# Kernel tuning notes

Hardware: AMD Instinct MI355X
Metric: run time of the kernel (lower is better)

Reference implementation:

```python
import jax, jax.numpy as jnp
import numpy as np

N_USERS = 100000
N_ITEMS = 50000
D = 64
N_LAYERS = 3
N_NODES = N_USERS + N_ITEMS + 1  # item table has padding row
N_EDGES = 4800000


def setup_inputs() -> dict:
    key = jax.random.key(0)
    k1, k2, k3, k4, k5 = jax.random.split(key, 5)
    user_emb = jax.random.normal(k1, (N_USERS, D), dtype=jnp.float32)
    item_emb = jax.random.normal(k2, (N_ITEMS + 1, D), dtype=jnp.float32)
    vals = jax.random.uniform(k3, (N_EDGES,), dtype=jnp.float32)
    rows = jax.random.randint(k4, (N_EDGES,), 0, N_NODES, dtype=jnp.int64)
    cols = jax.random.randint(k5, (N_EDGES,), 0, N_NODES, dtype=jnp.int64)
    return {"user_emb": user_emb, "item_emb": item_emb, "vals": vals,
            "rows": rows, "cols": cols}


def _spmm(rows, cols, vals, h):
    # y[r] = sum_{e: rows[e]==r} vals[e] * h[cols[e]]
    gathered = vals[:, None] * h[cols]                     # [E, D]
    return jax.ops.segment_sum(gathered, rows, num_segments=N_NODES)


def reference(user_emb, item_emb, vals, rows, cols):
    ego = jnp.concatenate([user_emb, item_emb], axis=0)    # [N, D]
    layer_embeddings = [ego]
    h = ego
    for _ in range(N_LAYERS):
        h = _spmm(rows, cols, vals, h)
        layer_embeddings.append(h)
    h_sum = jnp.stack(layer_embeddings, axis=0).sum(axis=0)
    return (h_sum, *layer_embeddings)
```

## Files before the change

### kernel.cpp

```cpp
#include <hip/hip_runtime.h>
#include <hip/hip_fp16.h>

#define N_USERS 100000
#define N_ITEMS 50000
#define DIM     64
#define N_NODES (N_USERS + N_ITEMS + 1)
#define N_EDGES 4800000

static constexpr long long NF = (long long)N_NODES * DIM;

#define NCB      256
#define CB_ROWS  586
#define CHUNK_E  8192
#define BINA_T   256
#define NCHUNK   ((N_EDGES + CHUNK_E - 1) / CHUNK_E)
#define PB_T     1024

__device__ __forceinline__ uint2 pack_half4(float4 s) {
    uint2 pk;
    *(__half2*)&pk.x = __float22half2_rn(make_float2(s.x, s.y));
    *(__half2*)&pk.y = __float22half2_rn(make_float2(s.z, s.w));
    return pk;
}

__global__ void concat16_kernel(const float4* __restrict__ user,
                                const float4* __restrict__ item,
                                float4* __restrict__ ego,
                                uint2* __restrict__ ego16) {
    int i = blockIdx.x * blockDim.x + threadIdx.x;
    const int userF4 = N_USERS * DIM / 4;
    const int totF4  = (int)(NF / 4);
    if (i < totF4) {
        float4 v = (i < userF4) ? user[i] : item[i - userF4];
        ego[i]   = v;
        ego16[i] = pack_half4(v);
    }
}

__global__ void concat_kernel(const float4* __restrict__ user,
                              const float4* __restrict__ item,
                              float4* __restrict__ ego) {
    int i = blockIdx.x * blockDim.x + threadIdx.x;
    const int userF4 = N_USERS * DIM / 4;
    const int totF4  = (int)(NF / 4);
    if (i < userF4)      ego[i] = user[i];
    else if (i < totF4)  ego[i] = item[i - userF4];
}

__global__ void __launch_bounds__(BINA_T)
binA_count_kernel(const int* __restrict__ rows, int* __restrict__ cnt) {
    __shared__ int hist[NCB];
    int t = threadIdx.x;
    int base = blockIdx.x * CHUNK_E;
    int nend = N_EDGES - base; if (nend > CHUNK_E) nend = CHUNK_E;
    hist[t] = 0;
    __syncthreads();
    for (int i = t; i < nend; i += BINA_T)
        atomicAdd(&hist[rows[base + i] / CB_ROWS], 1);
    __syncthreads();
    cnt[blockIdx.x * NCB + t] = hist[t];
}

__global__ void __launch_bounds__(BINA_T)
binA_scan_kernel(int* __restrict__ cnt, int* __restrict__ stored) {
    __shared__ int lds[BINA_T];
    int b = blockIdx.x, t = threadIdx.x;
    int w0 = 3 * t;
    int v0 = (w0     < NCHUNK) ? cnt[(w0    ) * NCB + b] : 0;
    int v1 = (w0 + 1 < NCHUNK) ? cnt[(w0 + 1) * NCB + b] : 0;
    int v2 = (w0 + 2 < NCHUNK) ? cnt[(w0 + 2) * NCB + b] : 0;
    lds[t] = v0 + v1 + v2;
    __syncthreads();
    for (int off = 1; off < BINA_T; off <<= 1) {
        int x = lds[t];
        int y = (t >= off) ? lds[t - off] : 0;
        __syncthreads();
        lds[t] = x + y;
        __syncthreads();
    }
    int excl = (t == 0) ? 0 : lds[t - 1];
    if (w0     < NCHUNK) cnt[(w0    ) * NCB + b] = excl;
    if (w0 + 1 < NCHUNK) cnt[(w0 + 1) * NCB + b] = excl + v0;
    if (w0 + 2 < NCHUNK) cnt[(w0 + 2) * NCB + b] = excl + v0 + v1;
    if (t == BINA_T - 1) stored[b] = lds[BINA_T - 1];
}

__global__ void __launch_bounds__(NCB)
cb_scan_kernel(const int* __restrict__ stored, int* __restrict__ csr_base,
               int* __restrict__ row_ptr) {
    __shared__ int lds[NCB];
    int t = threadIdx.x;
    lds[t] = stored[t];
    __syncthreads();
    for (int off = 1; off < NCB; off <<= 1) {
        int x = lds[t];
        int y = (t >= off) ? lds[t - off] : 0;
        __syncthreads();
        lds[t] = x + y;
        __syncthreads();
    }
    csr_base[t] = (t == 0) ? 0 : lds[t - 1];
    if (t == 0) { csr_base[NCB] = lds[NCB - 1]; row_ptr[N_NODES] = N_EDGES; }
}

__global__ void __launch_bounds__(BINA_T)
binA_write_kernel(const int* __restrict__ rows, const int* __restrict__ cols,
                  const float* __restrict__ vals,
                  const int* __restrict__ cnt, const int* __restrict__ csr_base,
                  uint2* __restrict__ tmp) {
    __shared__ int offs[NCB];
    int t = threadIdx.x;
    int base = blockIdx.x * CHUNK_E;
    int nend = N_EDGES - base; if (nend > CHUNK_E) nend = CHUNK_E;
    offs[t] = csr_base[t] + cnt[blockIdx.x * NCB + t];
    __syncthreads();
    for (int i = t; i < nend; i += BINA_T) {
        int e = base + i;
        int r = rows[e];
        unsigned c = (unsigned)cols[e];
        unsigned v = __float_as_uint(vals[e]);
        int b = r / CB_ROWS;
        int p = atomicAdd(&offs[b], 1);
        tmp[p] = make_uint2(((unsigned)(r - b * CB_ROWS) << 18) | c, v);
    }
}

__global__ void __launch_bounds__(PB_T)
passB_kernel(const int* __restrict__ csr_base, const uint2* __restrict__ tmp,
             uint2* __restrict__ edges, int* __restrict__ row_ptr) {
    __shared__ int sdeg[PB_T];
    __shared__ int scur[CB_ROWS];
    int b = blockIdx.x, t = threadIdx.x;
    int cb = csr_base[b];
    int n  = csr_base[b + 1] - cb;
    const uint2* tb = tmp + cb;
    sdeg[t] = 0;
    __syncthreads();
    for (int i = t; i < n; i += PB_T)
        atomicAdd(&sdeg[tb[i].x >> 18], 1);
    __syncthreads();
    for (int off = 1; off < PB_T; off <<= 1) {
        int x = sdeg[t];
        int y = (t >= off) ? sdeg[t - off] : 0;
        __syncthreads();
        sdeg[t] = x + y;
        __syncthreads();
    }
    int excl = (t == 0) ? 0 : sdeg[t - 1];
    int gr = b * CB_ROWS + t;
    if (t < CB_ROWS && gr < N_NODES) {
        row_ptr[gr] = cb + excl;
        scur[t] = cb + excl;
    }
    __syncthreads();
    for (int i = t; i < n; i += PB_T) {
        uint2 ed = tb[i];
        int p = atomicAdd(&scur[ed.x >> 18], 1);
        edges[p] = make_uint2(ed.x & 0x3FFFFu, ed.y);
    }
}

__device__ __forceinline__ void fma4(float4& a, float w, float4 v) {
    a.x += w * v.x; a.y += w * v.y; a.z += w * v.z; a.w += w * v.w;
}
__device__ __forceinline__ void fma16(float4& a, float w, uint2 u) {
    float2 lo = __half22float2(*(const __half2*)&u.x);
    float2 hi = __half22float2(*(const __half2*)&u.y);
    a.x += w * lo.x; a.y += w * lo.y; a.z += w * hi.x; a.w += w * hi.y;
}

__global__ void __launch_bounds__(256)
spmm16_kernel(const int* __restrict__ row_ptr,
              const uint2* __restrict__ edges,
              const uint2* __restrict__ hin16,
              float* __restrict__ hout,
              uint2* __restrict__ hout16) {
    int wave = (blockIdx.x * blockDim.x + threadIdx.x) >> 6;
    int lane = threadIdx.x & 63;
    if (wave >= N_NODES) return;
    int g  = lane >> 4;
    int dq = lane & 15;
    int start = row_ptr[wave];
    int end   = row_ptr[wave + 1];
    float4 a0 = make_float4(0.f, 0.f, 0.f, 0.f);
    float4 a1 = a0, a2 = a0, a3 = a0;
    int e = start;
    for (; e + 16 <= end; e += 16) {
        uint2 e0 = edges[e + g];
        uint2 e1 = edges[e + 4 + g];
        uint2 e2 = edges[e + 8 + g];
        uint2 e3 = edges[e + 12 + g];
        uint2 v0 = hin16[(int)e0.x * 16 + dq];
        uint2 v1 = hin16[(int)e1.x * 16 + dq];
        uint2 v2 = hin16[(int)e2.x * 16 + dq];
        uint2 v3 = hin16[(int)e3.x * 16 + dq];
        fma16(a0, __uint_as_float(e0.y), v0);
        fma16(a1, __uint_as_float(e1.y), v1);
        fma16(a2, __uint_as_float(e2.y), v2);
        fma16(a3, __uint_as_float(e3.y), v3);
    }
    for (; e < end; e += 4) {
        int ei = e + g;
        uint2 ed = (ei < end) ? edges[ei] : make_uint2(0u, 0u);
        uint2 v = hin16[(int)ed.x * 16 + dq];
        fma16(a0, __uint_as_float(ed.y), v);
    }
    float4 s = make_float4((a0.x + a1.x) + (a2.x + a3.x),
                           (a0.y + a1.y) + (a2.y + a3.y),
                           (a0.z + a1.z) + (a2.z + a3.z),
                           (a0.w + a1.w) + (a2.w + a3.w));
    s.x += __shfl_xor(s.x, 16); s.y += __shfl_xor(s.y, 16);
    s.z += __shfl_xor(s.z, 16); s.w += __shfl_xor(s.w, 16);
    s.x += __shfl_xor(s.x, 32); s.y += __shfl_xor(s.y, 32);
    s.z += __shfl_xor(s.z, 32); s.w += __shfl_xor(s.w, 32);
    if (g == 0) {
        int o = wave * 16 + dq;
        ((float4*)hout)[o] = s;
        hout16[o] = pack_half4(s);
    }
}

__global__ void __launch_bounds__(256)
spmm16_fused_kernel(const int* __restrict__ row_ptr,
                    const uint2* __restrict__ edges,
                    const uint2* __restrict__ hin16,
                    const float* __restrict__ ego,
                    const float* __restrict__ h1,
                    const float* __restrict__ h2,
                    float* __restrict__ h3,
                    float* __restrict__ hsum) {
    int wave = (blockIdx.x * blockDim.x + threadIdx.x) >> 6;
    int lane = threadIdx.x & 63;
    if (wave >= N_NODES) return;
    int g  = lane >> 4;
    int dq = lane & 15;
    int start = row_ptr[wave];
    int end   = row_ptr[wave + 1];
    float4 a0 = make_float4(0.f, 0.f, 0.f, 0.f);
    float4 a1 = a0, a2 = a0, a3 = a0;
    int e = start;
    for (; e + 16 <= end; e += 16) {
        uint2 e0 = edges[e + g];
        uint2 e1 = edges[e + 4 + g];
        uint2 e2 = edges[e + 8 + g];
        uint2 e3 = edges[e + 12 + g];
        uint2 v0 = hin16[(int)e0.x * 16 + dq];
        uint2 v1 = hin16[(int)e1.x * 16 + dq];
        uint2 v2 = hin16[(int)e2.x * 16 + dq];
        uint2 v3 = hin16[(int)e3.x * 16 + dq];
        fma16(a0, __uint_as_float(e0.y), v0);
        fma16(a1, __uint_as_float(e1.y), v1);
        fma16(a2, __uint_as_float(e2.y), v2);
        fma16(a3, __uint_as_float(e3.y), v3);
    }
    for (; e < end; e += 4) {
        int ei = e + g;
        uint2 ed = (ei < end) ? edges[ei] : make_uint2(0u, 0u);
        uint2 v = hin16[(int)ed.x * 16 + dq];
        fma16(a0, __uint_as_float(ed.y), v);
    }
    float4 s = make_float4((a0.x + a1.x) + (a2.x + a3.x),
                           (a0.y + a1.y) + (a2.y + a3.y),
                           (a0.z + a1.z) + (a2.z + a3.z),
                           (a0.w + a1.w) + (a2.w + a3.w));
    s.x += __shfl_xor(s.x, 16); s.y += __shfl_xor(s.y, 16);
    s.z += __shfl_xor(s.z, 16); s.w += __shfl_xor(s.w, 16);
    s.x += __shfl_xor(s.x, 32); s.y += __shfl_xor(s.y, 32);
    s.z += __shfl_xor(s.z, 32); s.w += __shfl_xor(s.w, 32);
    if (g == 0) {
        int o = wave * 16 + dq;
        float4 E  = ((const float4*)ego)[o];
        float4 H1 = ((const float4*)h1)[o];
        float4 H2 = ((const float4*)h2)[o];
        ((float4*)h3)[o] = s;
        ((float4*)hsum)[o] = make_float4(E.x + H1.x + H2.x + s.x,
                                         E.y + H1.y + H2.y + s.y,
                                         E.z + H1.z + H2.z + s.z,
                                         E.w + H1.w + H2.w + s.w);
    }
}

__global__ void __launch_bounds__(256)
spmm_csr_kernel(const int* __restrict__ row_ptr,
                const uint2* __restrict__ edges,
                const float* __restrict__ hin,
                float* __restrict__ hout) {
    int wave = (blockIdx.x * blockDim.x + threadIdx.x) >> 6;
    int lane = threadIdx.x & 63;
    if (wave >= N_NODES) return;
    int g  = lane >> 4;
    int dq = lane & 15;
    const float4* __restrict__ hin4 = (const float4*)hin;
    int start = row_ptr[wave];
    int end   = row_ptr[wave + 1];
    float4 a0 = make_float4(0.f, 0.f, 0.f, 0.f);
    float4 a1 = a0, a2 = a0, a3 = a0;
    int e = start;
    for (; e + 16 <= end; e += 16) {
        uint2 e0 = edges[e + g];
        uint2 e1 = edges[e + 4 + g];
        uint2 e2 = edges[e + 8 + g];
        uint2 e3 = edges[e + 12 + g];
        float4 v0 = hin4[(int)e0.x * 16 + dq];
        float4 v1 = hin4[(int)e1.x * 16 + dq];
        float4 v2 = hin4[(int)e2.x * 16 + dq];
        float4 v3 = hin4[(int)e3.x * 16 + dq];
        fma4(a0, __uint_as_float(e0.y), v0);
        fma4(a1, __uint_as_float(e1.y), v1);
        fma4(a2, __uint_as_float(e2.y), v2);
        fma4(a3, __uint_as_float(e3.y), v3);
    }
    for (; e < end; e += 4) {
        int ei = e + g;
        uint2 ed = (ei < end) ? edges[ei] : make_uint2(0u, 0u);
        float4 v = hin4[(int)ed.x * 16 + dq];
        fma4(a0, __uint_as_float(ed.y), v);
    }
    float4 s = make_float4((a0.x + a1.x) + (a2.x + a3.x),
                           (a0.y + a1.y) + (a2.y + a3.y),
                           (a0.z + a1.z) + (a2.z + a3.z),
                           (a0.w + a1.w) + (a2.w + a3.w));
    s.x += __shfl_xor(s.x, 16); s.y += __shfl_xor(s.y, 16);
    s.z += __shfl_xor(s.z, 16); s.w += __shfl_xor(s.w, 16);
    s.x += __shfl_xor(s.x, 32); s.y += __shfl_xor(s.y, 32);
    s.z += __shfl_xor(s.z, 32); s.w += __shfl_xor(s.w, 32);
    if (g == 0) ((float4*)hout)[wave * 16 + dq] = s;
}

__global__ void __launch_bounds__(256)
spmm_csr_fused_kernel(const int* __restrict__ row_ptr,
                      const uint2* __restrict__ edges,
                      const float* __restrict__ h2,
                      const float* __restrict__ ego,
                      const float* __restrict__ h1,
                      float* __restrict__ h3,
                      float* __restrict__ hsum) {
    int wave = (blockIdx.x * blockDim.x + threadIdx.x) >> 6;
    int lane = threadIdx.x & 63;
    if (wave >= N_NODES) return;
    int g  = lane >> 4;
    int dq = lane & 15;
    const float4* __restrict__ h24 = (const float4*)h2;
    int start = row_ptr[wave];
    int end   = row_ptr[wave + 1];
    float4 a0 = make_float4(0.f, 0.f, 0.f, 0.f);
    float4 a1 = a0, a2 = a0, a3 = a0;
    int e = start;
    for (; e + 16 <= end; e += 16) {
        uint2 e0 = edges[e + g];
        uint2 e1 = edges[e + 4 + g];
        uint2 e2 = edges[e + 8 + g];
        uint2 e3 = edges[e + 12 + g];
        float4 v0 = h24[(int)e0.x * 16 + dq];
        float4 v1 = h24[(int)e1.x * 16 + dq];
        float4 v2 = h24[(int)e2.x * 16 + dq];
        float4 v3 = h24[(int)e3.x * 16 + dq];
        fma4(a0, __uint_as_float(e0.y), v0);
        fma4(a1, __uint_as_float(e1.y), v1);
        fma4(a2, __uint_as_float(e2.y), v2);
        fma4(a3, __uint_as_float(e3.y), v3);
    }
    for (; e < end; e += 4) {
        int ei = e + g;
        uint2 ed = (ei < end) ? edges[ei] : make_uint2(0u, 0u);
        float4 v = h24[(int)ed.x * 16 + dq];
        fma4(a0, __uint_as_float(ed.y), v);
    }
    float4 s = make_float4((a0.x + a1.x) + (a2.x + a3.x),
                           (a0.y + a1.y) + (a2.y + a3.y),
                           (a0.z + a1.z) + (a2.z + a3.z),
                           (a0.w + a1.w) + (a2.w + a3.w));
    s.x += __shfl_xor(s.x, 16); s.y += __shfl_xor(s.y, 16);
    s.z += __shfl_xor(s.z, 16); s.w += __shfl_xor(s.w, 16);
    s.x += __shfl_xor(s.x, 32); s.y += __shfl_xor(s.y, 32);
    s.z += __shfl_xor(s.z, 32); s.w += __shfl_xor(s.w, 32);
    if (g == 0) {
        int o = wave * 16 + dq;
        float4 E  = ((const float4*)ego)[o];
        float4 H1 = ((const float4*)h1)[o];
        float4 H2 = ((const float4*)h2)[o];
        ((float4*)h3)[o] = s;
        ((float4*)hsum)[o] = make_float4(E.x + H1.x + H2.x + s.x,
                                         E.y + H1.y + H2.y + s.y,
                                         E.z + H1.z + H2.z + s.z,
                                         E.w + H1.w + H2.w + s.w);
    }
}

__global__ void spmm_atomic_kernel(const int* __restrict__ rows,
                                   const int* __restrict__ cols,
                                   const float* __restrict__ vals,
                                   const float* __restrict__ hin,
                                   float* __restrict__ hout) {
    int e = blockIdx.x * 4 + (threadIdx.x >> 6);
    int d = threadIdx.x & 63;
    if (e < N_EDGES) {
        atomicAdd(&hout[rows[e] * DIM + d], vals[e] * hin[cols[e] * DIM + d]);
    }
}

__global__ void zero_f_kernel(float* __restrict__ p, long long n) {
    long long i = (long long)blockIdx.x * blockDim.x + threadIdx.x;
    if (i < n) p[i] = 0.f;
}

__global__ void sum_kernel(const float4* __restrict__ a,
                           const float4* __restrict__ b,
                           const float4* __restrict__ c,
                           const float4* __restrict__ d,
                           float4* __restrict__ out) {
    int i = blockIdx.x * blockDim.x + threadIdx.x;
    if (i < (int)(NF / 4)) {
        float4 x = a[i], y = b[i], z = c[i], w = d[i];
        out[i] = make_float4(x.x + y.x + z.x + w.x,
                             x.y + y.y + z.y + w.y,
                             x.z + y.z + z.z + w.z,
                             x.w + y.w + z.w + w.w);
    }
}

extern "C" void kernel_launch(void* const* d_in, const int* in_sizes, int n_in,
                              void* d_out, int out_size, void* d_ws, size_t ws_size,
                              hipStream_t stream) {
    const float* user = (const float*)d_in[0];
    const float* item = (const float*)d_in[1];
    const float* vals = (const float*)d_in[2];
    const int*   rows = (const int*)d_in[3];
    const int*   cols = (const int*)d_in[4];

    float* out  = (float*)d_out;
    float* hsum = out;
    float* ego  = out + NF;
    float* h1   = out + 2 * NF;
    float* h2   = out + 3 * NF;
    float* h3   = out + 4 * NF;

    const int totF4 = (int)(NF / 4);

    const size_t edgesB = (size_t)N_EDGES * 8;
    const size_t h16B   = (size_t)N_NODES * DIM * 2;
    const size_t intsB  = ((size_t)NCHUNK * NCB + (size_t)N_NODES + 2
                           + NCB + NCB + 2 + 16) * 4;
    const size_t need32 = edgesB + intsB;
    const size_t need16 = edgesB + 2 * h16B + intsB;

    if (ws_size >= need32) {
        uint2* edges = (uint2*)d_ws;
        char*  p     = (char*)(edges + N_EDGES);
        uint2* hA    = nullptr;
        uint2* hB    = nullptr;
        bool   f16   = (ws_size >= need16);
        if (f16) {
            hA = (uint2*)p;  p += h16B;
            hB = (uint2*)p;  p += h16B;
        }
        int* cnt      = (int*)p;
        int* row_ptr  = cnt + (size_t)NCHUNK * NCB;
        int* stored   = row_ptr + (N_NODES + 2);
        int* csr_base = stored + NCB;
        uint2* tmp    = (uint2*)h1;

        if (f16) {
            concat16_kernel<<<(totF4 + 255) / 256, 256, 0, stream>>>(
                (const float4*)user, (const float4*)item, (float4*)ego, hA);
        } else {
            concat_kernel<<<(totF4 + 255) / 256, 256, 0, stream>>>(
                (const float4*)user, (const float4*)item, (float4*)ego);
        }

        binA_count_kernel<<<NCHUNK, BINA_T, 0, stream>>>(rows, cnt);
        binA_scan_kernel<<<NCB, BINA_T, 0, stream>>>(cnt, stored);
        cb_scan_kernel<<<1, NCB, 0, stream>>>(stored, csr_base, row_ptr);
        binA_write_kernel<<<NCHUNK, BINA_T, 0, stream>>>(
            rows, cols, vals, cnt, csr_base, tmp);
        passB_kernel<<<NCB, PB_T, 0, stream>>>(csr_base, tmp, edges, row_ptr);

        const int spmmBlocks = (N_NODES * 64 + 255) / 256;
        if (f16) {
            spmm16_kernel<<<spmmBlocks, 256, 0, stream>>>(row_ptr, edges, hA, h1, hB);
            spmm16_kernel<<<spmmBlocks, 256, 0, stream>>>(row_ptr, edges, hB, h2, hA);
            spmm16_fused_kernel<<<spmmBlocks, 256, 0, stream>>>(
                row_ptr, edges, hA, ego, h1, h2, h3, hsum);
        } else {
            spmm_csr_kernel<<<spmmBlocks, 256, 0, stream>>>(row_ptr, edges, ego, h1);
            spmm_csr_kernel<<<spmmBlocks, 256, 0, stream>>>(row_ptr, edges, h1,  h2);
            spmm_csr_fused_kernel<<<spmmBlocks, 256, 0, stream>>>(
                row_ptr, edges, h2, ego, h1, h3, hsum);
        }
    } else {
        concat_kernel<<<(totF4 + 255) / 256, 256, 0, stream>>>(
            (const float4*)user, (const float4*)item, (float4*)ego);
        const long long nz = 3 * NF;
        zero_f_kernel<<<(int)((nz + 255) / 256), 256, 0, stream>>>(h1, nz);
        const int ablocks = (N_EDGES + 3) / 4;
        spmm_atomic_kernel<<<ablocks, 256, 0, stream>>>(rows, cols, vals, ego, h1);
        spmm_atomic_kernel<<<ablocks, 256, 0, stream>>>(rows, cols, vals, h1,  h2);
        spmm_atomic_kernel<<<ablocks, 256, 0, stream>>>(rows, cols, vals, h2,  h3);
        sum_kernel<<<(totF4 + 255) / 256, 256, 0, stream>>>(
            (const float4*)ego, (const float4*)h1, (const float4*)h2, (const float4*)h3,
            (float4*)hsum);
    }
}
```

Before: 702.0 us.

## Fuse concat into histogram kernel, drop cb_scan, use wave-shuffle scans

Merges the concat/fp16 pack kernel into the bin-count kernel as extra blocks and removes the separate single-block cb_scan launch. Bucket bases are now recomputed locally in the write and passB kernels. LDS Hillis-Steele scans are replaced with wave shuffle scans, CHUNK_E is halved to 4096 (more count blocks, CPT=5 per-thread scan), and explicit fmaf is used in fma16. The aim is fewer launches and cheaper preprocessing scans, at the cost of some redundant per-block prefix work and a larger count array.

```diff
diff --git a/kernel.cpp b/kernel.cpp
--- a/kernel.cpp
+++ b/kernel.cpp
@@ -11,10 +11,12 @@
 
 #define NCB      256
 #define CB_ROWS  586
-#define CHUNK_E  8192
+#define CHUNK_E  4096
 #define BINA_T   256
 #define NCHUNK   ((N_EDGES + CHUNK_E - 1) / CHUNK_E)
+#define CPT      5
 #define PB_T     1024
+#define CONCAT_BLK ((int)((NF / 4 + 255) / 256))
 
 __device__ __forceinline__ uint2 pack_half4(float4 s) {
     uint2 pk;
@@ -23,97 +25,88 @@
     return pk;
 }
 
-__global__ void concat16_kernel(const float4* __restrict__ user,
-                                const float4* __restrict__ item,
-                                float4* __restrict__ ego,
-                                uint2* __restrict__ ego16) {
-    int i = blockIdx.x * blockDim.x + threadIdx.x;
-    const int userF4 = N_USERS * DIM / 4;
-    const int totF4  = (int)(NF / 4);
-    if (i < totF4) {
-        float4 v = (i < userF4) ? user[i] : item[i - userF4];
-        ego[i]   = v;
-        ego16[i] = pack_half4(v);
-    }
-}
-
-__global__ void concat_kernel(const float4* __restrict__ user,
-                              const float4* __restrict__ item,
-                              float4* __restrict__ ego) {
-    int i = blockIdx.x * blockDim.x + threadIdx.x;
-    const int userF4 = N_USERS * DIM / 4;
-    const int totF4  = (int)(NF / 4);
-    if (i < userF4)      ego[i] = user[i];
-    else if (i < totF4)  ego[i] = item[i - userF4];
+__device__ __forceinline__ int wavescan256_excl(int own, int t, int* wp) {
+    int lane = t & 63, wid = t >> 6;
+    int v = own;
+    #pragma unroll
+    for (int off = 1; off < 64; off <<= 1) {
+        int y = __shfl_up(v, off);
+        if (lane >= off) v += y;
+    }
+    if (lane == 63) wp[wid] = v;
+    __syncthreads();
+    int woff = 0;
+    #pragma unroll
+    for (int w = 0; w < 4; ++w) if (w < wid) woff += wp[w];
+    return v + woff - own;
 }
 
 __global__ void __launch_bounds__(BINA_T)
-binA_count_kernel(const int* __restrict__ rows, int* __restrict__ cnt) {
+fused_count_concat_kernel(const int* __restrict__ rows, int* __restrict__ cnt,
+                          const float4* __restrict__ user,
+                          const float4* __restrict__ item,
+                          float4* __restrict__ ego, uint2* __restrict__ ego16) {
     __shared__ int hist[NCB];
-    int t = threadIdx.x;
-    int base = blockIdx.x * CHUNK_E;
-    int nend = N_EDGES - base; if (nend > CHUNK_E) nend = CHUNK_E;
-    hist[t] = 0;
-    __syncthreads();
-    for (int i = t; i < nend; i += BINA_T)
-        atomicAdd(&hist[rows[base + i] / CB_ROWS], 1);
-    __syncthreads();
-    cnt[blockIdx.x * NCB + t] = hist[t];
+    int bb = blockIdx.x;
+    int t  = threadIdx.x;
+    if (bb < NCHUNK) {
+        hist[t] = 0;
+        __syncthreads();
+        int base = bb * CHUNK_E;
+        int nend = N_EDGES - base; if (nend > CHUNK_E) nend = CHUNK_E;
+        for (int i = t; i < nend; i += BINA_T)
+            atomicAdd(&hist[rows[base + i] / CB_ROWS], 1);
+        __syncthreads();
+        cnt[bb * NCB + t] = hist[t];
+    } else {
+        int i = (bb - NCHUNK) * BINA_T + t;
+        const int userF4 = N_USERS * DIM / 4;
+        const int totF4  = (int)(NF / 4);
+        if (i < totF4) {
+            float4 v = (i < userF4) ? user[i] : item[i - userF4];
+            ego[i] = v;
+            if (ego16) ego16[i] = pack_half4(v);
+        }
+    }
 }
 
 __global__ void __launch_bounds__(BINA_T)
 binA_scan_kernel(int* __restrict__ cnt, int* __restrict__ stored) {
-    __shared__ int lds[BINA_T];
+    __shared__ int wp[4];
     int b = blockIdx.x, t = threadIdx.x;
-    int w0 = 3 * t;
-    int v0 = (w0     < NCHUNK) ? cnt[(w0    ) * NCB + b] : 0;
-    int v1 = (w0 + 1 < NCHUNK) ? cnt[(w0 + 1) * NCB + b] : 0;
-    int v2 = (w0 + 2 < NCHUNK) ? cnt[(w0 + 2) * NCB + b] : 0;
-    lds[t] = v0 + v1 + v2;
-    __syncthreads();
-    for (int off = 1; off < BINA_T; off <<= 1) {
-        int x = lds[t];
-        int y = (t >= off) ? lds[t - off] : 0;
-        __syncthreads();
-        lds[t] = x + y;
-        __syncthreads();
-    }
-    int excl = (t == 0) ? 0 : lds[t - 1];
-    if (w0     < NCHUNK) cnt[(w0    ) * NCB + b] = excl;
-    if (w0 + 1 < NCHUNK) cnt[(w0 + 1) * NCB + b] = excl + v0;
-    if (w0 + 2 < NCHUNK) cnt[(w0 + 2) * NCB + b] = excl + v0 + v1;
-    if (t == BINA_T - 1) stored[b] = lds[BINA_T - 1];
-}
-
-__global__ void __launch_bounds__(NCB)
-cb_scan_kernel(const int* __restrict__ stored, int* __restrict__ csr_base,
-               int* __restrict__ row_ptr) {
-    __shared__ int lds[NCB];
-    int t = threadIdx.x;
-    lds[t] = stored[t];
-    __syncthreads();
-    for (int off = 1; off < NCB; off <<= 1) {
-        int x = lds[t];
-        int y = (t >= off) ? lds[t - off] : 0;
-        __syncthreads();
-        lds[t] = x + y;
-        __syncthreads();
-    }
-    csr_base[t] = (t == 0) ? 0 : lds[t - 1];
-    if (t == 0) { csr_base[NCB] = lds[NCB - 1]; row_ptr[N_NODES] = N_EDGES; }
+    int v[CPT];
+    int s = 0;
+    #pragma unroll
+    for (int i = 0; i < CPT; ++i) {
+        int idx = CPT * t + i;
+        int x = (idx < NCHUNK) ? cnt[idx * NCB + b] : 0;
+        v[i] = s;
+        s += x;
+    }
+    int excl = wavescan256_excl(s, t, wp);
+    #pragma unroll
+    for (int i = 0; i < CPT; ++i) {
+        int idx = CPT * t + i;
+        if (idx < NCHUNK) cnt[idx * NCB + b] = excl + v[i];
+    }
+    if (t == BINA_T - 1) stored[b] = excl + s;
 }
 
 __global__ void __launch_bounds__(BINA_T)
 binA_write_kernel(const int* __restrict__ rows, const int* __restrict__ cols,
                   const float* __restrict__ vals,
-                  const int* __restrict__ cnt, const int* __restrict__ csr_base,
+                  const int* __restrict__ cnt, const int* __restrict__ stored,
                   uint2* __restrict__ tmp) {
     __shared__ int offs[NCB];
+    __shared__ int wp[4];
     int t = threadIdx.x;
-    int base = blockIdx.x * CHUNK_E;
+    int bb = blockIdx.x;
+    int sv = stored[t];
+    int csr_b = wavescan256_excl(sv, t, wp);
+    offs[t] = csr_b + cnt[bb * NCB + t];
+    __syncthreads();
+    int base = bb * CHUNK_E;
     int nend = N_EDGES - base; if (nend > CHUNK_E) nend = CHUNK_E;
-    offs[t] = csr_base[t] + cnt[blockIdx.x * NCB + t];
-    __syncthreads();
     for (int i = t; i < nend; i += BINA_T) {
         int e = base + i;
         int r = rows[e];
@@ -126,32 +119,43 @@
 }
 
 __global__ void __launch_bounds__(PB_T)
-passB_kernel(const int* __restrict__ csr_base, const uint2* __restrict__ tmp,
+passB_kernel(const int* __restrict__ stored, const uint2* __restrict__ tmp,
              uint2* __restrict__ edges, int* __restrict__ row_ptr) {
     __shared__ int sdeg[PB_T];
     __shared__ int scur[CB_ROWS];
+    __shared__ int wp16[16];
+    __shared__ int cbs;
     int b = blockIdx.x, t = threadIdx.x;
-    int cb = csr_base[b];
-    int n  = csr_base[b + 1] - cb;
+    if (t == 0) cbs = 0;
+    sdeg[t] = 0;
+    __syncthreads();
+    if (t < b) atomicAdd(&cbs, stored[t]);
+    __syncthreads();
+    int cb = cbs;
+    int n  = stored[b];
     const uint2* tb = tmp + cb;
-    sdeg[t] = 0;
-    __syncthreads();
     for (int i = t; i < n; i += PB_T)
         atomicAdd(&sdeg[tb[i].x >> 18], 1);
     __syncthreads();
-    for (int off = 1; off < PB_T; off <<= 1) {
-        int x = sdeg[t];
-        int y = (t >= off) ? sdeg[t - off] : 0;
-        __syncthreads();
-        sdeg[t] = x + y;
-        __syncthreads();
-    }
-    int excl = (t == 0) ? 0 : sdeg[t - 1];
+    int own = sdeg[t];
+    int lane = t & 63, wid = t >> 6;
+    int v = own;
+    #pragma unroll
+    for (int off = 1; off < 64; off <<= 1) {
+        int y = __shfl_up(v, off);
+        if (lane >= off) v += y;
+    }
+    if (lane == 63) wp16[wid] = v;
+    __syncthreads();
+    int woff = 0;
+    for (int w = 0; w < wid; ++w) woff += wp16[w];
+    int excl = v + woff - own;
     int gr = b * CB_ROWS + t;
     if (t < CB_ROWS && gr < N_NODES) {
         row_ptr[gr] = cb + excl;
         scur[t] = cb + excl;
     }
+    if (b == 0 && t == 0) row_ptr[N_NODES] = N_EDGES;
     __syncthreads();
     for (int i = t; i < n; i += PB_T) {
         uint2 ed = tb[i];
@@ -166,7 +170,8 @@
 __device__ __forceinline__ void fma16(float4& a, float w, uint2 u) {
     float2 lo = __half22float2(*(const __half2*)&u.x);
     float2 hi = __half22float2(*(const __half2*)&u.y);
-    a.x += w * lo.x; a.y += w * lo.y; a.z += w * hi.x; a.w += w * hi.y;
+    a.x = fmaf(w, lo.x, a.x); a.y = fmaf(w, lo.y, a.y);
+    a.z = fmaf(w, hi.x, a.z); a.w = fmaf(w, hi.y, a.w);
 }
 
 __global__ void __launch_bounds__(256)
@@ -404,6 +409,16 @@
     if (i < n) p[i] = 0.f;
 }
 
+__global__ void concat_kernel(const float4* __restrict__ user,
+                              const float4* __restrict__ item,
+                              float4* __restrict__ ego) {
+    int i = blockIdx.x * blockDim.x + threadIdx.x;
+    const int userF4 = N_USERS * DIM / 4;
+    const int totF4  = (int)(NF / 4);
+    if (i < userF4)      ego[i] = user[i];
+    else if (i < totF4)  ego[i] = item[i - userF4];
+}
+
 __global__ void sum_kernel(const float4* __restrict__ a,
                            const float4* __restrict__ b,
                            const float4* __restrict__ c,
@@ -440,7 +455,7 @@
     const size_t edgesB = (size_t)N_EDGES * 8;
     const size_t h16B   = (size_t)N_NODES * DIM * 2;
     const size_t intsB  = ((size_t)NCHUNK * NCB + (size_t)N_NODES + 2
-                           + NCB + NCB + 2 + 16) * 4;
+                           + NCB + 16) * 4;
     const size_t need32 = edgesB + intsB;
     const size_t need16 = edgesB + 2 * h16B + intsB;
 
@@ -454,26 +469,18 @@
             hA = (uint2*)p;  p += h16B;
             hB = (uint2*)p;  p += h16B;
         }
-        int* cnt      = (int*)p;
-        int* row_ptr  = cnt + (size_t)NCHUNK * NCB;
-        int* stored   = row_ptr + (N_NODES + 2);
-        int* csr_base = stored + NCB;
-        uint2* tmp    = (uint2*)h1;
-
-        if (f16) {
-            concat16_kernel<<<(totF4 + 255) / 256, 256, 0, stream>>>(
-                (const float4*)user, (const float4*)item, (float4*)ego, hA);
-        } else {
-            concat_kernel<<<(totF4 + 255) / 256, 256, 0, stream>>>(
-                (const float4*)user, (const float4*)item, (float4*)ego);
-        }
-
-        binA_count_kernel<<<NCHUNK, BINA_T, 0, stream>>>(rows, cnt);
+        int* cnt     = (int*)p;
+        int* row_ptr = cnt + (size_t)NCHUNK * NCB;
+        int* stored  = row_ptr + (N_NODES + 2);
+        uint2* tmp   = (uint2*)h1;
+
+        fused_count_concat_kernel<<<NCHUNK + CONCAT_BLK, BINA_T, 0, stream>>>(
+            rows, cnt, (const float4*)user, (const float4*)item,
+            (float4*)ego, hA);
         binA_scan_kernel<<<NCB, BINA_T, 0, stream>>>(cnt, stored);
-        cb_scan_kernel<<<1, NCB, 0, stream>>>(stored, csr_base, row_ptr);
         binA_write_kernel<<<NCHUNK, BINA_T, 0, stream>>>(
-            rows, cols, vals, cnt, csr_base, tmp);
-        passB_kernel<<<NCB, PB_T, 0, stream>>>(csr_base, tmp, edges, row_ptr);
+            rows, cols, vals, cnt, stored, tmp);
+        passB_kernel<<<NCB, PB_T, 0, stream>>>(stored, tmp, edges, row_ptr);
 
         const int spmmBlocks = (N_NODES * 64 + 255) / 256;
         if (f16) {
```

Result: no change. 688.5 us (-1.9%).
